# Optimization experiments

Measured on AMD Instinct MI355X. Metric: run time of the kernel, lower is better.

Reference implementation:

```python
import jax, jax.numpy as jnp
import numpy as np

B, D = 500000, 128
UNITS, STACK, NPRED = 4, 12, 2
EPS = 1e-3  # Keras BatchNormalization default epsilon


def setup_inputs() -> dict:
    key = jax.random.key(0)
    ks = jax.random.split(key, 2 * STACK + 4)
    inp = {"x": jax.random.normal(ks[0], (B, D), dtype=jnp.float32)}
    # 12 dense weights with growing input width D + 4*i
    for i in range(STACK):
        inp[f"w{i}"] = jax.random.normal(ks[1 + i], (D + UNITS * i, UNITS), dtype=jnp.float32) * 0.1
    inp["gamma"] = 1.0 + 0.1 * jax.random.normal(ks[STACK + 1], (STACK, UNITS), dtype=jnp.float32)
    inp["beta"] = 0.1 * jax.random.normal(ks[STACK + 2], (STACK, UNITS), dtype=jnp.float32)
    inp["mean"] = 0.1 * jax.random.normal(ks[STACK + 3], (STACK, UNITS), dtype=jnp.float32)
    inp["var"] = 0.5 + jax.random.uniform(ks[2 * STACK], (STACK, UNITS), dtype=jnp.float32)
    inp["wf"] = jax.random.normal(ks[2 * STACK + 1], (D + UNITS * STACK, NPRED), dtype=jnp.float32) * 0.1
    inp["bf"] = jnp.zeros((NPRED,), dtype=jnp.float32)
    return inp


def reference(x, w0, w1, w2, w3, w4, w5, w6, w7, w8, w9, w10, w11,
              gamma, beta, mean, var, wf, bf):
    ws = [w0, w1, w2, w3, w4, w5, w6, w7, w8, w9, w10, w11]
    h = x
    for i in range(STACK):
        y = h @ ws[i]  # [B, 4]
        # inference-mode BatchNorm, fused scale/shift
        scale = gamma[i] * jax.lax.rsqrt(var[i] + EPS)
        y = jax.nn.relu(y * scale + (beta[i] - mean[i] * scale))
        h = jnp.concatenate([y, h], axis=-1)  # width grows by 4
    logits = h @ wf + bf  # [B, 2]
    return jax.nn.softmax(logits, axis=-1)
```

## Files before the change

kernel.cpp:

```cpp
#include <hip/hip_runtime.h>

#define NROWS 500000
#define DD 128
#define NSTACK 12
#define BNEPS 1e-3f
#define NCOL 50
#define TRS 50

typedef float  v2f    __attribute__((ext_vector_type(2)));
typedef float  v4f    __attribute__((ext_vector_type(4)));
typedef float  f32x4  __attribute__((ext_vector_type(4)));
typedef __bf16 bf16x8 __attribute__((ext_vector_type(8)));

__device__ __forceinline__ unsigned short f2bf_rn(float f) {
    unsigned u = __float_as_uint(f);
    return (unsigned short)((u + 0x7FFFu + ((u >> 16) & 1u)) >> 16);
}

__global__ __launch_bounds__(256, 2) void predict_kernel(
    const float* __restrict__ x,
    const float* __restrict__ w0,  const float* __restrict__ w1,
    const float* __restrict__ w2,  const float* __restrict__ w3,
    const float* __restrict__ w4,  const float* __restrict__ w5,
    const float* __restrict__ w6,  const float* __restrict__ w7,
    const float* __restrict__ w8,  const float* __restrict__ w9,
    const float* __restrict__ w10, const float* __restrict__ w11,
    const float* __restrict__ gamma_, const float* __restrict__ beta_,
    const float* __restrict__ mean_,  const float* __restrict__ var_,
    const float* __restrict__ wf,     const float* __restrict__ bf,
    float* __restrict__ out)
{
    __shared__ __align__(16) union {
        unsigned short bsw[4][4][64][8];
        float          trow[256 * TRS];
    } sh;
    __shared__ __align__(16) float SC[48];
    __shared__ __align__(16) float SH[48];
    __shared__ float BF2[2];

    const int tid = threadIdx.x;
    const float* ws[NSTACK] = {w0,w1,w2,w3,w4,w5,w6,w7,w8,w9,w10,w11};

    for (int idx = tid; idx < 1024; idx += 256)
        ((f32x4*)&sh.bsw[0][0][0][0])[idx] = (f32x4){0.f, 0.f, 0.f, 0.f};
    __syncthreads();

#pragma unroll
    for (int i = 0; i < NSTACK; ++i) {
        const float* wsi = ws[i];
        for (int e = tid; e < 512; e += 256) {
            const int k = e >> 2, u = e & 3;
            const int n = 4 * i + u;
            const int kt = k >> 5, q = (k >> 3) & 3, j = k & 7;
            const int nt = n >> 4, lane = q * 16 + (n & 15);
            sh.bsw[kt][nt][lane][j] = f2bf_rn(wsi[16 * i + e]);
        }
    }
    {
        const int e = tid;
        const int k = e >> 1, u = e & 1;
        const int n = 48 + u;
        const int kt = k >> 5, q = (k >> 3) & 3, j = k & 7;
        const int lane = q * 16 + (n & 15);
        sh.bsw[kt][3][lane][j] = f2bf_rn(wf[96 + e]);
    }
    if (tid < 48) {
        const float sc = gamma_[tid] * __frsqrt_rn(var_[tid] + BNEPS);
        SC[tid] = sc;
        SH[tid] = beta_[tid] - mean_[tid] * sc;
    }
    if (tid < 2) BF2[tid] = bf[tid];
    __syncthreads();

    const int lane = tid & 63;
    const int wv   = tid >> 6;
    const int rowbase = blockIdx.x * 256 + wv * 64;
    const int m = lane & 15;
    const int q = lane >> 4;

    const float* arow[4];
#pragma unroll
    for (int mt = 0; mt < 4; ++mt) {
        int r = rowbase + mt * 16 + m;
        if (r > NROWS - 1) r = NROWS - 1;
        arow[mt] = x + (size_t)r * DD + q * 8;
    }

    f32x4 acc[4][4];
#pragma unroll
    for (int mt = 0; mt < 4; ++mt)
#pragma unroll
        for (int nt = 0; nt < 4; ++nt) acc[mt][nt] = (f32x4){0.f, 0.f, 0.f, 0.f};

#pragma unroll
    for (int kt = 0; kt < 4; ++kt) {
        bf16x8 bfrag[4];
#pragma unroll
        for (int nt = 0; nt < 4; ++nt)
            bfrag[nt] = *(const bf16x8*)&sh.bsw[kt][nt][lane][0];
#pragma unroll
        for (int mt = 0; mt < 4; ++mt) {
            const v4f a0 = *(const v4f*)(arow[mt] + kt * 32);
            const v4f a1 = *(const v4f*)(arow[mt] + kt * 32 + 4);
            union { unsigned short us[8]; bf16x8 bv; } au;
#pragma unroll
            for (int e = 0; e < 4; ++e) {
                au.us[e]     = f2bf_rn(a0[e]);
                au.us[4 + e] = f2bf_rn(a1[e]);
            }
#pragma unroll
            for (int nt = 0; nt < 4; ++nt)
                acc[mt][nt] = __builtin_amdgcn_mfma_f32_16x16x32_bf16(
                    au.bv, bfrag[nt], acc[mt][nt], 0, 0, 0);
        }
    }

    __syncthreads();

    float* tr = &sh.trow[wv * 64 * TRS];
#pragma unroll
    for (int mt = 0; mt < 4; ++mt)
#pragma unroll
        for (int nt = 0; nt < 4; ++nt) {
            const int c = nt * 16 + m;
            if (c < NCOL) {
#pragma unroll
                for (int r = 0; r < 4; ++r)
                    tr[(mt * 16 + q * 4 + r) * TRS + c] = acc[mt][nt][r];
            }
        }

    const float* myT = &sh.trow[(wv * 64 + lane) * TRS];
    float T[NCOL];
#pragma unroll
    for (int j = 0; j < NCOL / 2; ++j) {
        const v2f t = *(const v2f*)(myT + 2 * j);
        T[2 * j] = t.x; T[2 * j + 1] = t.y;
    }

    float y[NSTACK * 4];
#pragma unroll
    for (int i = 0; i < NSTACK; ++i) {
        float a0 = T[4 * i + 0], a1 = T[4 * i + 1];
        float a2 = T[4 * i + 2], a3 = T[4 * i + 3];
        const float* wsi = ws[i];
#pragma unroll
        for (int mr = 0; mr < 4 * i; ++mr) {
            const float hv = y[(i - 1 - (mr >> 2)) * 4 + (mr & 3)];
            a0 += hv * wsi[4 * mr + 0];
            a1 += hv * wsi[4 * mr + 1];
            a2 += hv * wsi[4 * mr + 2];
            a3 += hv * wsi[4 * mr + 3];
        }
        const v4f scv = *(const v4f*)&SC[4 * i];
        const v4f shv = *(const v4f*)&SH[4 * i];
        const float r0 = a0 * scv.x + shv.x;
        const float r1 = a1 * scv.y + shv.y;
        const float r2 = a2 * scv.z + shv.z;
        const float r3 = a3 * scv.w + shv.w;
        y[4 * i + 0] = r0 > 0.f ? r0 : 0.f;
        y[4 * i + 1] = r1 > 0.f ? r1 : 0.f;
        y[4 * i + 2] = r2 > 0.f ? r2 : 0.f;
        y[4 * i + 3] = r3 > 0.f ? r3 : 0.f;
    }

    float l0 = T[48] + BF2[0];
    float l1 = T[49] + BF2[1];
#pragma unroll
    for (int mr = 0; mr < 48; ++mr) {
        const float hv = y[(11 - (mr >> 2)) * 4 + (mr & 3)];
        l0 += hv * wf[2 * mr + 0];
        l1 += hv * wf[2 * mr + 1];
    }

    const float mx = fmaxf(l0, l1);
    const float e0 = __expf(l0 - mx);
    const float e1 = __expf(l1 - mx);
    const float inv = 1.0f / (e0 + e1);

    const int row = rowbase + lane;
    if (row < NROWS)
        *(v2f*)(out + (size_t)row * 2) = (v2f){e0 * inv, e1 * inv};
}

extern "C" void kernel_launch(void* const* d_in, const int* in_sizes, int n_in,
                              void* d_out, int out_size, void* d_ws, size_t ws_size,
                              hipStream_t stream) {
    const float* x   = (const float*)d_in[0];
    const float* w0  = (const float*)d_in[1];
    const float* w1  = (const float*)d_in[2];
    const float* w2  = (const float*)d_in[3];
    const float* w3  = (const float*)d_in[4];
    const float* w4  = (const float*)d_in[5];
    const float* w5  = (const float*)d_in[6];
    const float* w6  = (const float*)d_in[7];
    const float* w7  = (const float*)d_in[8];
    const float* w8  = (const float*)d_in[9];
    const float* w9  = (const float*)d_in[10];
    const float* w10 = (const float*)d_in[11];
    const float* w11 = (const float*)d_in[12];
    const float* gm  = (const float*)d_in[13];
    const float* bt  = (const float*)d_in[14];
    const float* mn  = (const float*)d_in[15];
    const float* vr  = (const float*)d_in[16];
    const float* wf  = (const float*)d_in[17];
    const float* bf  = (const float*)d_in[18];
    float* out = (float*)d_out;

    dim3 block(256);
    dim3 grid((NROWS + 255) / 256);
    hipLaunchKernelGGL(predict_kernel, grid, block, 0, stream,
                       x, w0, w1, w2, w3, w4, w5, w6, w7, w8, w9, w10, w11,
                       gm, bt, mn, vr, wf, bf, out);
}
```

Measured before the change: 417.5 us.

## Move weight fragment packing and BN folding into a separate prep kernel

```diff
diff --git a/kernel.cpp b/kernel.cpp
--- a/kernel.cpp
+++ b/kernel.cpp
@@ -17,8 +17,8 @@
     return (unsigned short)((u + 0x7FFFu + ((u >> 16) & 1u)) >> 16);
 }
 
-__global__ __launch_bounds__(256, 2) void predict_kernel(
-    const float* __restrict__ x,
+
+__global__ void prep_kernel(
     const float* __restrict__ w0,  const float* __restrict__ w1,
     const float* __restrict__ w2,  const float* __restrict__ w3,
     const float* __restrict__ w4,  const float* __restrict__ w5,
@@ -27,51 +27,55 @@
     const float* __restrict__ w10, const float* __restrict__ w11,
     const float* __restrict__ gamma_, const float* __restrict__ beta_,
     const float* __restrict__ mean_,  const float* __restrict__ var_,
-    const float* __restrict__ wf,     const float* __restrict__ bf,
+    const float* __restrict__ wf,     const float* __restrict__ bfv,
+    unsigned short* __restrict__ frag, float* __restrict__ sc,
+    float* __restrict__ sh, float* __restrict__ bf2)
+{
+    const float* ws[NSTACK] = {w0,w1,w2,w3,w4,w5,w6,w7,w8,w9,w10,w11};
+    const int f    = blockIdx.x * 256 + threadIdx.x;
+    const int j    = f & 7;
+    const int lane = (f >> 3) & 63;
+    const int nt   = (f >> 9) & 3;
+    const int kt   = f >> 11;
+    const int k    = kt * 32 + (lane >> 4) * 8 + j;
+    const int n    = nt * 16 + (lane & 15);
+
+    float val = 0.f;
+    if (n < 48) {
+        const int i = n >> 2, u = n & 3;
+        val = ws[i][16 * i + 4 * k + u];
+    } else if (n < NCOL) {
+        val = wf[96 + 2 * k + (n - 48)];
+    }
+    frag[f] = f2bf_rn(val);
+
+    if (blockIdx.x == 0) {
+        if (threadIdx.x < 48) {
+            const float s = gamma_[threadIdx.x] * __frsqrt_rn(var_[threadIdx.x] + BNEPS);
+            sc[threadIdx.x] = s;
+            sh[threadIdx.x] = beta_[threadIdx.x] - mean_[threadIdx.x] * s;
+        }
+        if (threadIdx.x < 2) bf2[threadIdx.x] = bfv[threadIdx.x];
+    }
+}
+
+__global__ __launch_bounds__(256, 3) void predict_kernel(
+    const float* __restrict__ x,
+    const float* __restrict__ w0,  const float* __restrict__ w1,
+    const float* __restrict__ w2,  const float* __restrict__ w3,
+    const float* __restrict__ w4,  const float* __restrict__ w5,
+    const float* __restrict__ w6,  const float* __restrict__ w7,
+    const float* __restrict__ w8,  const float* __restrict__ w9,
+    const float* __restrict__ w10, const float* __restrict__ w11,
+    const float* __restrict__ wf,
+    const unsigned short* __restrict__ frag,
+    const float* __restrict__ SCg, const float* __restrict__ SHg,
+    const float* __restrict__ BFg,
     float* __restrict__ out)
 {
-    __shared__ __align__(16) union {
-        unsigned short bsw[4][4][64][8];
-        float          trow[256 * TRS];
-    } sh;
-    __shared__ __align__(16) float SC[48];
-    __shared__ __align__(16) float SH[48];
-    __shared__ float BF2[2];
-
-    const int tid = threadIdx.x;
-    const float* ws[NSTACK] = {w0,w1,w2,w3,w4,w5,w6,w7,w8,w9,w10,w11};
-
-    for (int idx = tid; idx < 1024; idx += 256)
-        ((f32x4*)&sh.bsw[0][0][0][0])[idx] = (f32x4){0.f, 0.f, 0.f, 0.f};
-    __syncthreads();
-
-#pragma unroll
-    for (int i = 0; i < NSTACK; ++i) {
-        const float* wsi = ws[i];
-        for (int e = tid; e < 512; e += 256) {
-            const int k = e >> 2, u = e & 3;
-            const int n = 4 * i + u;
-            const int kt = k >> 5, q = (k >> 3) & 3, j = k & 7;
-            const int nt = n >> 4, lane = q * 16 + (n & 15);
-            sh.bsw[kt][nt][lane][j] = f2bf_rn(wsi[16 * i + e]);
-        }
-    }
-    {
-        const int e = tid;
-        const int k = e >> 1, u = e & 1;
-        const int n = 48 + u;
-        const int kt = k >> 5, q = (k >> 3) & 3, j = k & 7;
-        const int lane = q * 16 + (n & 15);
-        sh.bsw[kt][3][lane][j] = f2bf_rn(wf[96 + e]);
-    }
-    if (tid < 48) {
-        const float sc = gamma_[tid] * __frsqrt_rn(var_[tid] + BNEPS);
-        SC[tid] = sc;
-        SH[tid] = beta_[tid] - mean_[tid] * sc;
-    }
-    if (tid < 2) BF2[tid] = bf[tid];
-    __syncthreads();
-
+    __shared__ __align__(16) float trow[256 * TRS];
+
+    const int tid  = threadIdx.x;
     const int lane = tid & 63;
     const int wv   = tid >> 6;
     const int rowbase = blockIdx.x * 256 + wv * 64;
@@ -97,27 +101,25 @@
         bf16x8 bfrag[4];
 #pragma unroll
         for (int nt = 0; nt < 4; ++nt)
-            bfrag[nt] = *(const bf16x8*)&sh.bsw[kt][nt][lane][0];
+            bfrag[nt] = *(const bf16x8*)(frag + (((kt * 4 + nt) * 64 + lane) << 3));
 #pragma unroll
         for (int mt = 0; mt < 4; ++mt) {
             const v4f a0 = *(const v4f*)(arow[mt] + kt * 32);
             const v4f a1 = *(const v4f*)(arow[mt] + kt * 32 + 4);
-            union { unsigned short us[8]; bf16x8 bv; } au;
+            bf16x8 av;
 #pragma unroll
             for (int e = 0; e < 4; ++e) {
-                au.us[e]     = f2bf_rn(a0[e]);
-                au.us[4 + e] = f2bf_rn(a1[e]);
+                av[e]     = (__bf16)a0[e];
+                av[4 + e] = (__bf16)a1[e];
             }
 #pragma unroll
             for (int nt = 0; nt < 4; ++nt)
                 acc[mt][nt] = __builtin_amdgcn_mfma_f32_16x16x32_bf16(
-                    au.bv, bfrag[nt], acc[mt][nt], 0, 0, 0);
-        }
-    }
-
-    __syncthreads();
-
-    float* tr = &sh.trow[wv * 64 * TRS];
+                    av, bfrag[nt], acc[mt][nt], 0, 0, 0);
+        }
+    }
+
+    float* tr = &trow[wv * 64 * TRS];
 #pragma unroll
     for (int mt = 0; mt < 4; ++mt)
 #pragma unroll
@@ -130,19 +132,15 @@
             }
         }
 
-    const float* myT = &sh.trow[(wv * 64 + lane) * TRS];
-    float T[NCOL];
-#pragma unroll
-    for (int j = 0; j < NCOL / 2; ++j) {
-        const v2f t = *(const v2f*)(myT + 2 * j);
-        T[2 * j] = t.x; T[2 * j + 1] = t.y;
-    }
+    const float* myT = &trow[(wv * 64 + lane) * TRS];
+    const float* ws[NSTACK] = {w0,w1,w2,w3,w4,w5,w6,w7,w8,w9,w10,w11};
 
     float y[NSTACK * 4];
 #pragma unroll
     for (int i = 0; i < NSTACK; ++i) {
-        float a0 = T[4 * i + 0], a1 = T[4 * i + 1];
-        float a2 = T[4 * i + 2], a3 = T[4 * i + 3];
+        const v2f t0 = *(const v2f*)(myT + 4 * i);
+        const v2f t1 = *(const v2f*)(myT + 4 * i + 2);
+        float a0 = t0.x, a1 = t0.y, a2 = t1.x, a3 = t1.y;
         const float* wsi = ws[i];
 #pragma unroll
         for (int mr = 0; mr < 4 * i; ++mr) {
@@ -152,8 +150,8 @@
             a2 += hv * wsi[4 * mr + 2];
             a3 += hv * wsi[4 * mr + 3];
         }
-        const v4f scv = *(const v4f*)&SC[4 * i];
-        const v4f shv = *(const v4f*)&SH[4 * i];
+        const v4f scv = *(const v4f*)(SCg + 4 * i);
+        const v4f shv = *(const v4f*)(SHg + 4 * i);
         const float r0 = a0 * scv.x + shv.x;
         const float r1 = a1 * scv.y + shv.y;
         const float r2 = a2 * scv.z + shv.z;
@@ -164,8 +162,9 @@
         y[4 * i + 3] = r3 > 0.f ? r3 : 0.f;
     }
 
-    float l0 = T[48] + BF2[0];
-    float l1 = T[49] + BF2[1];
+    const v2f tl = *(const v2f*)(myT + 48);
+    float l0 = tl.x + BFg[0];
+    float l1 = tl.y + BFg[1];
 #pragma unroll
     for (int mr = 0; mr < 48; ++mr) {
         const float hv = y[(11 - (mr >> 2)) * 4 + (mr & 3)];
@@ -207,9 +206,18 @@
     const float* bf  = (const float*)d_in[18];
     float* out = (float*)d_out;
 
+    unsigned short* frag = (unsigned short*)d_ws;
+    float* SCg = (float*)((char*)d_ws + 16384);
+    float* SHg = (float*)((char*)d_ws + 16576);
+    float* BFg = (float*)((char*)d_ws + 16768);
+
+    hipLaunchKernelGGL(prep_kernel, dim3(32), dim3(256), 0, stream,
+                       w0, w1, w2, w3, w4, w5, w6, w7, w8, w9, w10, w11,
+                       gm, bt, mn, vr, wf, bf, frag, SCg, SHg, BFg);
+
     dim3 block(256);
     dim3 grid((NROWS + 255) / 256);
     hipLaunchKernelGGL(predict_kernel, grid, block, 0, stream,
                        x, w0, w1, w2, w3, w4, w5, w6, w7, w8, w9, w10, w11,
-                       gm, bt, mn, vr, wf, bf, out);
-}
+                       wf, frag, SCg, SHg, BFg, out);
+}
```

Measured after the change: 396.6 us. 5.0% less time.
